# Optimization experiments

Measured on AMD Instinct MI355X. Metric: run time of the kernel, lower is better.

The kernel has to match this reference:

```python
import jax, jax.numpy as jnp
from jax import lax
import numpy as np

TOP_PERCENT = 1.3
KSIZE = 3
SIGMA = 0.3 * ((KSIZE - 1) * 0.5 - 1) + 0.8  # torchvision default sigma for ksize=3 -> 0.8


def _gaussian_kernel1d():
    x = jnp.arange(KSIZE, dtype=jnp.float32) - (KSIZE - 1) / 2.0
    k = jnp.exp(-0.5 * (x / SIGMA) ** 2)
    return k / k.sum()


def setup_inputs() -> dict:
    key = jax.random.key(0)
    img = jax.random.uniform(key, (3, 4096, 4096), dtype=jnp.float32)
    return {"img": img}


def reference(img):
    # --- rgb_to_grayscale (ITU-R 601 coefficients, as torchvision) ---
    gray = 0.2989 * img[0] + 0.587 * img[1] + 0.114 * img[2]  # [H, W]

    # --- separable 3x3 gaussian blur, reflect padding (torchvision) ---
    k = _gaussian_kernel1d()
    p = jnp.pad(gray, 1, mode="reflect")  # [H+2, W+2]
    # horizontal pass
    h = k[0] * p[:, :-2] + k[1] * p[:, 1:-1] + k[2] * p[:, 2:]  # [H+2, W]
    # vertical pass
    blur = k[0] * h[:-2, :] + k[1] * h[1:-1, :] + k[2] * h[2:, :]  # [H, W]

    # --- quantile threshold (linear interpolation, matches torch.quantile) ---
    q = (100.0 - TOP_PERCENT) / 100.0
    threshold = jnp.quantile(blur, q)
    mask = (blur >= threshold).astype(jnp.int32)  # [H, W]

    # --- binary opening with 5x5 ones footprint ---
    # erosion = min filter; outside-image treated as 0 (scipy border_value=0),
    # so pad explicitly with zeros and reduce with VALID windows.
    INT_MAX = np.iinfo(np.int32).max
    INT_MIN = np.iinfo(np.int32).min
    padded = jnp.pad(mask, 2)  # zero pad -> borders erode
    eroded = lax.reduce_window(padded, INT_MAX, lax.min, (5, 5), (1, 1), "VALID")
    # dilation = max filter; identity padding (-inf equiv) matches border_value=0
    opened = lax.reduce_window(eroded, INT_MIN, lax.max, (5, 5), (1, 1), "SAME")

    return opened[None, :, :].astype(jnp.int32)  # [1, H, W]
```

## Files before the change

### kernel.cpp

```cpp
#include <hip/hip_runtime.h>
#include <stdint.h>
#include <cmath>


#define HH 4096
#define WW 4096
#define KRANK 16559111u
#define CAP 65536u

__device__ __forceinline__ unsigned ukey(float v) {
  return (unsigned)(v * 268435456.0f);
}
__device__ __forceinline__ int refl(int i) {
  return i < 0 ? -i : (i > 4095 ? 8190 - i : i);
}
__device__ __forceinline__ float grayf(float r, float g, float b) {
  return __fadd_rn(__fadd_rn(__fmul_rn(0.2989f, r), __fmul_rn(0.587f, g)),
                   __fmul_rn(0.114f, b));
}
__device__ __forceinline__ float tap3(float a, float b, float c, float kn0, float kn1) {
  return __fadd_rn(__fadd_rn(__fmul_rn(kn0, a), __fmul_rn(kn1, b)),
                   __fmul_rn(kn0, c));
}

__global__ __launch_bounds__(512) void k_blur(const float* __restrict__ img,
    float4* __restrict__ blur4, unsigned* __restrict__ hist1,
    float kn0, float kn1) {
  __shared__ unsigned hist[4096];
  const int tid = threadIdx.x;
  #pragma unroll
  for (int i = tid; i < 4096; i += 512) hist[i] = 0u;
  __syncthreads();

  const int lane = tid & 63, wv = tid >> 6;
  const int bc = (blockIdx.x & 15) << 8;
  const int r0 = (blockIdx.x >> 4) << 6;
  const int rstart = r0 + (wv << 3);
  const float* __restrict__ Rp = img;
  const float* __restrict__ Gp = img + 16777216;
  const float* __restrict__ Bp = img + 33554432;
  const int c4 = bc + (lane << 2);
  const int colL = (bc == 0) ? 1 : bc - 1;
  const int colR = (bc == 3840) ? 4094 : bc + 256;
  const int hc = (lane == 0) ? colL : ((lane == 63) ? colR : c4);

  auto hrow = [&](int r) -> float4 {
    const size_t base = ((size_t)refl(r) << 12);
    float4 R = *(const float4*)(Rp + base + c4);
    float4 G = *(const float4*)(Gp + base + c4);
    float4 B = *(const float4*)(Bp + base + c4);
    float hr = Rp[base + hc], hg = Gp[base + hc], hb = Bp[base + hc];
    float4 g;
    g.x = grayf(R.x, G.x, B.x);
    g.y = grayf(R.y, G.y, B.y);
    g.z = grayf(R.z, G.z, B.z);
    g.w = grayf(R.w, G.w, B.w);
    float ghalo = grayf(hr, hg, hb);
    float gl = __shfl_up(g.w, 1);
    float gr_ = __shfl_down(g.x, 1);
    gl = (lane == 0) ? ghalo : gl;
    gr_ = (lane == 63) ? ghalo : gr_;
    float4 h;
    h.x = tap3(gl, g.x, g.y, kn0, kn1);
    h.y = tap3(g.x, g.y, g.z, kn0, kn1);
    h.z = tap3(g.y, g.z, g.w, kn0, kn1);
    h.w = tap3(g.z, g.w, gr_, kn0, kn1);
    return h;
  };

  float4 h0 = hrow(rstart - 1);
  float4 h1 = hrow(rstart);
  #pragma unroll
  for (int i = 0; i < 8; ++i) {
    float4 h2 = hrow(rstart + 1 + i);
    float4 v;
    v.x = tap3(h0.x, h1.x, h2.x, kn0, kn1);
    v.y = tap3(h0.y, h1.y, h2.y, kn0, kn1);
    v.z = tap3(h0.z, h1.z, h2.z, kn0, kn1);
    v.w = tap3(h0.w, h1.w, h2.w, kn0, kn1);
    blur4[(((size_t)(rstart + i) << 12) + c4) >> 2] = v;
    atomicAdd(&hist[ukey(v.x) >> 16], 1u);
    atomicAdd(&hist[ukey(v.y) >> 16], 1u);
    atomicAdd(&hist[ukey(v.z) >> 16], 1u);
    atomicAdd(&hist[ukey(v.w) >> 16], 1u);
    h0 = h1; h1 = h2;
  }
  __syncthreads();
  #pragma unroll
  for (int i = tid; i < 4096; i += 512) {
    unsigned c = hist[i];
    if (c) atomicAdd(&hist1[i], c);
  }
}

__global__ __launch_bounds__(256) void k_sel1(const unsigned* __restrict__ hist1,
                                              unsigned* __restrict__ sel) {
  __shared__ unsigned part[256];
  const int t = threadIdx.x;
  unsigned loc[16];
  unsigned s = 0;
  for (int i = 0; i < 16; ++i) { loc[i] = hist1[t * 16 + i]; s += loc[i]; }
  part[t] = s;
  __syncthreads();
  for (int off = 1; off < 256; off <<= 1) {
    unsigned v = (t >= off) ? part[t - off] : 0u;
    __syncthreads();
    part[t] += v;
    __syncthreads();
  }
  unsigned incl = part[t], excl = incl - s;
  if (excl <= KRANK && KRANK < incl) {
    unsigned p = excl;
    for (int i = 0; i < 16; ++i) {
      if (KRANK < p + loc[i]) { sel[0] = (unsigned)(t * 16 + i); sel[1] = KRANK - p; break; }
      p += loc[i];
    }
  }
}

__global__ __launch_bounds__(256) void k_pass2(const float* __restrict__ blur,
    const unsigned* __restrict__ sel, unsigned* __restrict__ hist2,
    unsigned* __restrict__ cnt, unsigned long long* __restrict__ list,
    unsigned long long* __restrict__ mbits) {
  __shared__ unsigned lcnt, lbase;
  __shared__ unsigned lidx[256];
  __shared__ unsigned short lkey[256];
  if (threadIdx.x == 0) lcnt = 0u;
  __syncthreads();
  const unsigned b1 = sel[0];
  const unsigned ub = (b1 + 1u) << 16;
  const unsigned base = blockIdx.x * 8192u + threadIdx.x;
  #pragma unroll 4
  for (int it = 0; it < 32; ++it) {
    unsigned i = base + (unsigned)it * 256u;
    unsigned u = ukey(blur[i]);
    unsigned long long w = __ballot(u >= ub);
    if ((threadIdx.x & 63) == 0) mbits[i >> 6] = w;
    if ((u >> 16) == b1) {
      atomicAdd(&hist2[u & 0xFFFFu], 1u);
      unsigned x = atomicAdd(&lcnt, 1u);
      if (x < 256u) { lidx[x] = i; lkey[x] = (unsigned short)(u & 0xFFFFu); }
      else {
        unsigned g = atomicAdd(cnt, 1u);
        if (g < CAP) list[g] = ((unsigned long long)i << 16) | (u & 0xFFFFu);
      }
    }
  }
  __syncthreads();
  unsigned n = lcnt > 256u ? 256u : lcnt;
  if (threadIdx.x == 0 && n) lbase = atomicAdd(cnt, n);
  __syncthreads();
  if (threadIdx.x < n) {
    unsigned g = lbase + threadIdx.x;
    if (g < CAP)
      list[g] = ((unsigned long long)lidx[threadIdx.x] << 16) | (unsigned)lkey[threadIdx.x];
  }
}

__global__ __launch_bounds__(1024) void k_sel2fix(const unsigned* __restrict__ hist2,
    const unsigned* __restrict__ sel, const unsigned* __restrict__ cnt,
    const unsigned long long* __restrict__ list,
    unsigned long long* __restrict__ mbits) {
  __shared__ unsigned part[1024];
  __shared__ unsigned sLo;
  const int t = threadIdx.x;
  const unsigned base = (unsigned)t * 64u;
  unsigned s = 0;
  for (int i = 0; i < 64; ++i) s += hist2[base + i];
  part[t] = s;
  __syncthreads();
  for (int off = 1; off < 1024; off <<= 1) {
    unsigned v = (t >= off) ? part[t - off] : 0u;
    __syncthreads();
    part[t] += v;
    __syncthreads();
  }
  unsigned incl = part[t], excl = incl - s;
  const unsigned r1 = sel[1];
  if (excl <= r1 && r1 < incl) {
    unsigned p = excl;
    for (int i = 0; i < 64; ++i) {
      unsigned c = hist2[base + i];
      if (r1 < p + c) { sLo = base + i; break; }
      p += c;
    }
  }
  __syncthreads();
  const unsigned lo = sLo;
  unsigned n = *cnt; if (n > CAP) n = CAP;
  for (unsigned j = t; j < n; j += 1024) {
    unsigned long long e = list[j];
    if ((unsigned)(e & 0xFFFFu) >= lo) {
      unsigned long long pix = e >> 16;
      atomicOr(&mbits[pix >> 6], 1ull << (pix & 63));
    }
  }
}

__global__ __launch_bounds__(256) void k_morph(
    const unsigned long long* __restrict__ mbits, int4* __restrict__ out4) {
  __shared__ unsigned long long er[12][64];
  __shared__ unsigned long long dl[8][64];
  const int r0 = blockIdx.x << 3;
  for (int t = threadIdx.x; t < 12 * 64; t += 256) {
    int lr = t >> 6, wc = t & 63;
    int rr = r0 - 2 + lr;
    unsigned long long acc = 0ull;
    if (rr >= 0 && rr < HH) {
      acc = ~0ull;
      #pragma unroll
      for (int dr = -2; dr <= 2; ++dr) {
        int mr = rr + dr;
        unsigned long long h = 0ull;
        if (mr >= 0 && mr < HH) {
          int rb = (mr << 6) + wc;
          unsigned long long C = mbits[rb];
          unsigned long long L = (wc > 0) ? mbits[rb - 1] : 0ull;
          unsigned long long R = (wc < 63) ? mbits[rb + 1] : 0ull;
          h = C & ((C >> 1) | (R << 63)) & ((C >> 2) | (R << 62))
                & ((C << 1) | (L >> 63)) & ((C << 2) | (L >> 62));
        }
        acc &= h;
      }
    }
    er[lr][wc] = acc;
  }
  __syncthreads();
  for (int t = threadIdx.x; t < 8 * 64; t += 256) {
    int lr = t >> 6, wc = t & 63;
    unsigned long long acc = 0ull;
    #pragma unroll
    for (int dr = 0; dr <= 4; ++dr) {
      unsigned long long C = er[lr + dr][wc];
      unsigned long long L = (wc > 0) ? er[lr + dr][wc - 1] : 0ull;
      unsigned long long R = (wc < 63) ? er[lr + dr][wc + 1] : 0ull;
      acc |= C | ((C >> 1) | (R << 63)) | ((C >> 2) | (R << 62))
               | ((C << 1) | (L >> 63)) | ((C << 2) | (L >> 62));
    }
    dl[lr][wc] = acc;
  }
  __syncthreads();
  const size_t p0 = (size_t)r0 << 10;
  for (int j = threadIdx.x; j < 8192; j += 256) {
    unsigned long long word = dl[j >> 10][(j >> 4) & 63];
    unsigned nib = (unsigned)(word >> ((j & 15) << 2)) & 0xFu;
    out4[p0 + j] = make_int4(nib & 1, (nib >> 1) & 1, (nib >> 2) & 1, (nib >> 3) & 1);
  }
}

extern "C" void kernel_launch(void* const* d_in, const int* in_sizes, int n_in,
                              void* d_out, int out_size, void* d_ws, size_t ws_size,
                              hipStream_t stream) {
  (void)in_sizes; (void)n_in; (void)out_size; (void)ws_size;
  const float* img = (const float*)d_in[0];
  char* ws = (char*)d_ws;

  float* blur = (float*)ws;
  unsigned* hist1 = (unsigned*)(ws + 67108864);
  unsigned* hist2 = (unsigned*)(ws + 67125248);
  unsigned* cnt   = (unsigned*)(ws + 67387392);
  unsigned* sel   = (unsigned*)(ws + 67387456);
  unsigned long long* list  = (unsigned long long*)(ws + 67387520);
  unsigned long long* mbits = (unsigned long long*)(ws + 67911808);

  float t = 1.0f / 0.8f;
  float k0 = expf(-0.5f * (t * t));
  float k1 = 1.0f;
  float s = (k0 + k1) + k0;
  float kn0 = k0 / s, kn1 = k1 / s;

  hipMemsetAsync(hist1, 0, 16384 + 262144 + 64, stream);
  k_blur<<<1024, 512, 0, stream>>>(img, (float4*)blur, hist1, kn0, kn1);
  k_sel1<<<1, 256, 0, stream>>>(hist1, sel);
  k_pass2<<<2048, 256, 0, stream>>>(blur, sel, hist2, cnt, list, mbits);
  k_sel2fix<<<1, 1024, 0, stream>>>(hist2, sel, cnt, list, mbits);
  k_morph<<<512, 256, 0, stream>>>(mbits, (int4*)d_out);
}
```

Measured before the change: 365.7 us.

## Retile blur kernel, use nontemporal stores/loads, vectorize histogram scan

Each blur wave now processes 16 rows instead of 8, with two waves per row band covering 512 columns. The grid is halved, launch bounds add an occupancy hint, and the fully unrolled loops are removed. The blur and final output writes and the pass2 blur reads use nontemporal builtins, meant to cut cache pollution on streaming traffic. k_sel2fix loads hist2 as uint4 into registers and reuses them instead of re-reading global memory. The workspace layout is reordered. Fewer vertical halo recomputations are traded against a longer serial loop and higher register pressure.

```diff
diff --git a/kernel.cpp b/kernel.cpp
--- a/kernel.cpp
+++ b/kernel.cpp
@@ -8,6 +8,9 @@
 #define KRANK 16559111u
 #define CAP 65536u
 
+typedef float  nfloat4 __attribute__((ext_vector_type(4)));
+typedef int    nint4   __attribute__((ext_vector_type(4)));
+
 __device__ __forceinline__ unsigned ukey(float v) {
   return (unsigned)(v * 268435456.0f);
 }
@@ -23,19 +26,17 @@
                    __fmul_rn(kn0, c));
 }
 
-__global__ __launch_bounds__(512) void k_blur(const float* __restrict__ img,
-    float4* __restrict__ blur4, unsigned* __restrict__ hist1,
+__global__ __launch_bounds__(512, 8) void k_blur(const float* __restrict__ img,
+    float* __restrict__ blur, unsigned* __restrict__ hist1,
     float kn0, float kn1) {
   __shared__ unsigned hist[4096];
   const int tid = threadIdx.x;
-  #pragma unroll
   for (int i = tid; i < 4096; i += 512) hist[i] = 0u;
   __syncthreads();
 
   const int lane = tid & 63, wv = tid >> 6;
-  const int bc = (blockIdx.x & 15) << 8;
-  const int r0 = (blockIdx.x >> 4) << 6;
-  const int rstart = r0 + (wv << 3);
+  const int bc = ((blockIdx.x & 7) << 9) + ((wv & 1) << 8);
+  const int rs = ((blockIdx.x >> 3) << 6) + ((wv >> 1) << 4);
   const float* __restrict__ Rp = img;
   const float* __restrict__ Gp = img + 16777216;
   const float* __restrict__ Bp = img + 33554432;
@@ -68,17 +69,17 @@
     return h;
   };
 
-  float4 h0 = hrow(rstart - 1);
-  float4 h1 = hrow(rstart);
-  #pragma unroll
-  for (int i = 0; i < 8; ++i) {
-    float4 h2 = hrow(rstart + 1 + i);
-    float4 v;
+  float4 h0 = hrow(rs - 1);
+  float4 h1 = hrow(rs);
+  for (int i = 0; i < 16; ++i) {
+    float4 h2 = hrow(rs + 1 + i);
+    nfloat4 v;
     v.x = tap3(h0.x, h1.x, h2.x, kn0, kn1);
     v.y = tap3(h0.y, h1.y, h2.y, kn0, kn1);
     v.z = tap3(h0.z, h1.z, h2.z, kn0, kn1);
     v.w = tap3(h0.w, h1.w, h2.w, kn0, kn1);
-    blur4[(((size_t)(rstart + i) << 12) + c4) >> 2] = v;
+    __builtin_nontemporal_store(
+        v, (nfloat4*)(blur + ((size_t)(rs + i) << 12) + c4));
     atomicAdd(&hist[ukey(v.x) >> 16], 1u);
     atomicAdd(&hist[ukey(v.y) >> 16], 1u);
     atomicAdd(&hist[ukey(v.z) >> 16], 1u);
@@ -86,7 +87,6 @@
     h0 = h1; h1 = h2;
   }
   __syncthreads();
-  #pragma unroll
   for (int i = tid; i < 4096; i += 512) {
     unsigned c = hist[i];
     if (c) atomicAdd(&hist1[i], c);
@@ -133,7 +133,7 @@
   #pragma unroll 4
   for (int it = 0; it < 32; ++it) {
     unsigned i = base + (unsigned)it * 256u;
-    unsigned u = ukey(blur[i]);
+    unsigned u = ukey(__builtin_nontemporal_load(&blur[i]));
     unsigned long long w = __ballot(u >= ub);
     if ((threadIdx.x & 63) == 0) mbits[i >> 6] = w;
     if ((u >> 16) == b1) {
@@ -164,9 +164,15 @@
   __shared__ unsigned part[1024];
   __shared__ unsigned sLo;
   const int t = threadIdx.x;
-  const unsigned base = (unsigned)t * 64u;
+  unsigned loc[64];
+  const uint4* h4 = (const uint4*)hist2;
   unsigned s = 0;
-  for (int i = 0; i < 64; ++i) s += hist2[base + i];
+  #pragma unroll
+  for (int j = 0; j < 16; ++j) {
+    uint4 q = h4[t * 16 + j];
+    loc[4 * j] = q.x; loc[4 * j + 1] = q.y; loc[4 * j + 2] = q.z; loc[4 * j + 3] = q.w;
+    s += q.x + q.y + q.z + q.w;
+  }
   part[t] = s;
   __syncthreads();
   for (int off = 1; off < 1024; off <<= 1) {
@@ -180,9 +186,8 @@
   if (excl <= r1 && r1 < incl) {
     unsigned p = excl;
     for (int i = 0; i < 64; ++i) {
-      unsigned c = hist2[base + i];
-      if (r1 < p + c) { sLo = base + i; break; }
-      p += c;
+      if (r1 < p + loc[i]) { sLo = (unsigned)t * 64u + i; break; }
+      p += loc[i];
     }
   }
   __syncthreads();
@@ -198,7 +203,7 @@
 }
 
 __global__ __launch_bounds__(256) void k_morph(
-    const unsigned long long* __restrict__ mbits, int4* __restrict__ out4) {
+    const unsigned long long* __restrict__ mbits, int* __restrict__ out) {
   __shared__ unsigned long long er[12][64];
   __shared__ unsigned long long dl[8][64];
   const int r0 = blockIdx.x << 3;
@@ -240,11 +245,14 @@
     dl[lr][wc] = acc;
   }
   __syncthreads();
-  const size_t p0 = (size_t)r0 << 10;
+  const size_t p0 = (size_t)r0 << 12;
   for (int j = threadIdx.x; j < 8192; j += 256) {
     unsigned long long word = dl[j >> 10][(j >> 4) & 63];
     unsigned nib = (unsigned)(word >> ((j & 15) << 2)) & 0xFu;
-    out4[p0 + j] = make_int4(nib & 1, (nib >> 1) & 1, (nib >> 2) & 1, (nib >> 3) & 1);
+    nint4 o;
+    o.x = (int)(nib & 1); o.y = (int)((nib >> 1) & 1);
+    o.z = (int)((nib >> 2) & 1); o.w = (int)((nib >> 3) & 1);
+    __builtin_nontemporal_store(o, (nint4*)(out + p0 + (size_t)j * 4));
   }
 }
 
@@ -256,12 +264,12 @@
   char* ws = (char*)d_ws;
 
   float* blur = (float*)ws;
-  unsigned* hist1 = (unsigned*)(ws + 67108864);
-  unsigned* hist2 = (unsigned*)(ws + 67125248);
-  unsigned* cnt   = (unsigned*)(ws + 67387392);
-  unsigned* sel   = (unsigned*)(ws + 67387456);
-  unsigned long long* list  = (unsigned long long*)(ws + 67387520);
-  unsigned long long* mbits = (unsigned long long*)(ws + 67911808);
+  unsigned long long* mbits = (unsigned long long*)(ws + 67108864);
+  unsigned* hist1 = (unsigned*)(ws + 69206016);
+  unsigned* hist2 = (unsigned*)(ws + 69222400);
+  unsigned* cnt   = (unsigned*)(ws + 69484544);
+  unsigned* sel   = (unsigned*)(ws + 69484608);
+  unsigned long long* list = (unsigned long long*)(ws + 69484672);
 
   float t = 1.0f / 0.8f;
   float k0 = expf(-0.5f * (t * t));
@@ -269,10 +277,10 @@
   float s = (k0 + k1) + k0;
   float kn0 = k0 / s, kn1 = k1 / s;
 
-  hipMemsetAsync(hist1, 0, 16384 + 262144 + 64, stream);
-  k_blur<<<1024, 512, 0, stream>>>(img, (float4*)blur, hist1, kn0, kn1);
+  (void)hipMemsetAsync(hist1, 0, 16384 + 262144 + 64, stream);
+  k_blur<<<512, 512, 0, stream>>>(img, blur, hist1, kn0, kn1);
   k_sel1<<<1, 256, 0, stream>>>(hist1, sel);
   k_pass2<<<2048, 256, 0, stream>>>(blur, sel, hist2, cnt, list, mbits);
   k_sel2fix<<<1, 1024, 0, stream>>>(hist2, sel, cnt, list, mbits);
-  k_morph<<<512, 256, 0, stream>>>(mbits, (int4*)d_out);
-}
+  k_morph<<<512, 256, 0, stream>>>(mbits, (int*)d_out);
+}
```

Result: no change. 368.5 us (+0.8%).
